# Performance work log

Measured on AMD Instinct MI355X. Metric: run time of the kernel, lower is better.

Reference implementation:

```python
import jax, jax.numpy as jnp
import numpy as np

TEM_PER_GROUP = 4  # arg_split: templates per argument type


def setup_inputs() -> dict:
    key = jax.random.key(0)
    k1, k2, k3, k4, k5 = jax.random.split(key, 5)
    B, L, D, S, G = 8, 4096, 768, 32, 16
    T = G * TEM_PER_GROUP
    return {
        "sen_embs": jax.random.normal(k1, (B, L, D), dtype=jnp.float32),
        "arg_embs": jax.random.normal(k2, (B, S, T, D), dtype=jnp.float32),
        "mask_type": jax.random.uniform(k3, (B, S, G), dtype=jnp.float32),
        "span_start": jax.random.randint(k4, (B, S), 0, 4000),
        "span_len": jax.random.randint(k5, (B, S), 1, 20),
        "offset": 10,
    }


def reference(sen_embs, arg_embs, mask_type, span_start, span_len, offset):
    B, L, D = sen_embs.shape
    _, S, T, _ = arg_embs.shape
    G = T // TEM_PER_GROUP
    # variable-length span gather + mean pool (sen_emb[max(0,s-off):e+1+off].mean(0))
    lo = jnp.maximum(span_start - offset, 0)                       # [B,S]
    hi = jnp.minimum(span_start + span_len + 1 + offset, L)       # [B,S]
    pos = jnp.arange(L)
    m = ((pos[None, None, :] >= lo[:, :, None]) &
         (pos[None, None, :] < hi[:, :, None])).astype(sen_embs.dtype)  # [B,S,L]
    cnt = jnp.maximum(m.sum(-1), 1.0)                              # [B,S]
    span = jnp.einsum('bsl,bld->bsd', m, sen_embs) / cnt[:, :, None]    # [B,S,D]
    # similarity (dis='ou'): -||arg - span||^2 over feature dim
    diff = arg_embs - span[:, :, None, :]                          # [B,S,T,D]
    logits = -(diff * diff).sum(-1)                                # [B,S,T]
    # segmented max over template groups (torch.split + max)
    logits = logits.reshape(B, S, G, TEM_PER_GROUP).max(-1)        # [B,S,G]
    return logits * mask_type
```

## Files before the change

### kernel.cpp

```cpp
#include <hip/hip_runtime.h>

constexpr int B   = 8;
constexpr int L   = 4096;
constexpr int D   = 768;
constexpr int S   = 32;
constexpr int G   = 16;
constexpr int TPG = 4;
constexpr int T   = G * TPG;

__global__ __launch_bounds__(256) void span_sim_kernel(
    const float* __restrict__ sen,
    const float* __restrict__ arg,
    const float* __restrict__ mask,
    const int*   __restrict__ sstart,
    const int*   __restrict__ slen,
    const int*   __restrict__ offp,
    float*       __restrict__ out)
{
    const int bs   = blockIdx.x;
    const int b    = bs / S;
    const int tid  = threadIdx.x;
    const int lane = tid & 63;
    const int wave = tid >> 6;

    const int offset = offp[0];
    const int st = sstart[bs];
    const int ln = slen[bs];
    int lo = st - offset;           if (lo < 0) lo = 0;
    int hi = st + ln + 1 + offset;  if (hi > L) hi = L;
    const int cnt = hi - lo;

    __shared__ float span[D];

    const float* srow = sen + ((size_t)b * L + lo) * D;
    float a0 = 0.f, a1 = 0.f, a2 = 0.f;
    #pragma unroll 4
    for (int r = 0; r < cnt; ++r) {
        const float* p = srow + (size_t)r * D;
        a0 += p[tid];
        a1 += p[tid + 256];
        a2 += p[tid + 512];
    }
    const float inv = 1.0f / (float)cnt;
    span[tid]       = a0 * inv;
    span[tid + 256] = a1 * inv;
    span[tid + 512] = a2 * inv;
    __syncthreads();

    const float4* sp4 = reinterpret_cast<const float4*>(span);
    const float4 s0 = sp4[lane];
    const float4 s1 = sp4[lane + 64];
    const float4 s2 = sp4[lane + 128];

    const float4* abase = reinterpret_cast<const float4*>(arg + (size_t)bs * T * D);
    float gmax[4];
    #pragma unroll
    for (int i = 0; i < 16; ++i) {
        const int t = wave * 16 + i;
        const float4* a4 = abase + (size_t)t * (D / 4);
        const float4 v0 = a4[lane];
        const float4 v1 = a4[lane + 64];
        const float4 v2 = a4[lane + 128];
        float d = 0.f, x;
        x = v0.x - s0.x; d += x * x;  x = v0.y - s0.y; d += x * x;
        x = v0.z - s0.z; d += x * x;  x = v0.w - s0.w; d += x * x;
        x = v1.x - s1.x; d += x * x;  x = v1.y - s1.y; d += x * x;
        x = v1.z - s1.z; d += x * x;  x = v1.w - s1.w; d += x * x;
        x = v2.x - s2.x; d += x * x;  x = v2.y - s2.y; d += x * x;
        x = v2.z - s2.z; d += x * x;  x = v2.w - s2.w; d += x * x;
        #pragma unroll
        for (int o = 32; o >= 1; o >>= 1) d += __shfl_xor(d, o, 64);
        const float lg = -d;
        const int j = i >> 2;
        if ((i & 3) == 0) gmax[j] = lg;
        else              gmax[j] = fmaxf(gmax[j], lg);
    }

    if (lane == 0) {
        float*       o  = out  + (size_t)bs * G + wave * 4;
        const float* mk = mask + (size_t)bs * G + wave * 4;
        o[0] = gmax[0] * mk[0];
        o[1] = gmax[1] * mk[1];
        o[2] = gmax[2] * mk[2];
        o[3] = gmax[3] * mk[3];
    }
}

extern "C" void kernel_launch(void* const* d_in, const int* in_sizes, int n_in,
                              void* d_out, int out_size, void* d_ws, size_t ws_size,
                              hipStream_t stream) {
    const float* sen    = (const float*)d_in[0];
    const float* arg    = (const float*)d_in[1];
    const float* mask   = (const float*)d_in[2];
    const int*   sstart = (const int*)d_in[3];
    const int*   slen   = (const int*)d_in[4];
    const int*   offp   = (const int*)d_in[5];
    float*       out    = (float*)d_out;

    span_sim_kernel<<<B * S, 256, 0, stream>>>(sen, arg, mask, sstart, slen, offp, out);
}
```

Before: 172.4 us.

## Use 1024-thread blocks, splitting span rows and templates across more waves

After: 171.4 us. No clear change (-0.6%).

```diff
diff --git a/kernel.cpp b/kernel.cpp
--- a/kernel.cpp
+++ b/kernel.cpp
@@ -8,7 +8,7 @@
 constexpr int TPG = 4;
 constexpr int T   = G * TPG;
 
-__global__ __launch_bounds__(256) void span_sim_kernel(
+__global__ __launch_bounds__(1024) void span_sim_kernel(
     const float* __restrict__ sen,
     const float* __restrict__ arg,
     const float* __restrict__ mask,
@@ -18,7 +18,7 @@
     float*       __restrict__ out)
 {
     const int bs   = blockIdx.x;
-    const int b    = bs / S;
+    const int b    = bs >> 5;
     const int tid  = threadIdx.x;
     const int lane = tid & 63;
     const int wave = tid >> 6;
@@ -30,21 +30,33 @@
     int hi = st + ln + 1 + offset;  if (hi > L) hi = L;
     const int cnt = hi - lo;
 
+    __shared__ float part[4][D];
     __shared__ float span[D];
 
+    const int c  = tid & 255;
+    const int rq = tid >> 8;
     const float* srow = sen + ((size_t)b * L + lo) * D;
     float a0 = 0.f, a1 = 0.f, a2 = 0.f;
     #pragma unroll 4
-    for (int r = 0; r < cnt; ++r) {
+    for (int r = rq; r < cnt; r += 4) {
         const float* p = srow + (size_t)r * D;
-        a0 += p[tid];
-        a1 += p[tid + 256];
-        a2 += p[tid + 512];
+        a0 += p[c];
+        a1 += p[c + 256];
+        a2 += p[c + 512];
     }
-    const float inv = 1.0f / (float)cnt;
-    span[tid]       = a0 * inv;
-    span[tid + 256] = a1 * inv;
-    span[tid + 512] = a2 * inv;
+    part[rq][c]       = a0;
+    part[rq][c + 256] = a1;
+    part[rq][c + 512] = a2;
+    __syncthreads();
+
+    if (tid < 256) {
+        const float inv = 1.0f / (float)cnt;
+        #pragma unroll
+        for (int k = 0; k < 3; ++k) {
+            const int j = tid + k * 256;
+            span[j] = (part[0][j] + part[1][j] + part[2][j] + part[3][j]) * inv;
+        }
+    }
     __syncthreads();
 
     const float4* sp4 = reinterpret_cast<const float4*>(span);
@@ -53,11 +65,10 @@
     const float4 s2 = sp4[lane + 128];
 
     const float4* abase = reinterpret_cast<const float4*>(arg + (size_t)bs * T * D);
-    float gmax[4];
+    float dist[4];
     #pragma unroll
-    for (int i = 0; i < 16; ++i) {
-        const int t = wave * 16 + i;
-        const float4* a4 = abase + (size_t)t * (D / 4);
+    for (int i = 0; i < 4; ++i) {
+        const float4* a4 = abase + (size_t)(wave * 4 + i) * (D / 4);
         const float4 v0 = a4[lane];
         const float4 v1 = a4[lane + 64];
         const float4 v2 = a4[lane + 128];
@@ -68,21 +79,16 @@
         x = v1.z - s1.z; d += x * x;  x = v1.w - s1.w; d += x * x;
         x = v2.x - s2.x; d += x * x;  x = v2.y - s2.y; d += x * x;
         x = v2.z - s2.z; d += x * x;  x = v2.w - s2.w; d += x * x;
+        dist[i] = d;
+    }
+    #pragma unroll
+    for (int o = 32; o >= 1; o >>= 1) {
         #pragma unroll
-        for (int o = 32; o >= 1; o >>= 1) d += __shfl_xor(d, o, 64);
-        const float lg = -d;
-        const int j = i >> 2;
-        if ((i & 3) == 0) gmax[j] = lg;
-        else              gmax[j] = fmaxf(gmax[j], lg);
+        for (int i = 0; i < 4; ++i) dist[i] += __shfl_xor(dist[i], o, 64);
     }
-
     if (lane == 0) {
-        float*       o  = out  + (size_t)bs * G + wave * 4;
-        const float* mk = mask + (size_t)bs * G + wave * 4;
-        o[0] = gmax[0] * mk[0];
-        o[1] = gmax[1] * mk[1];
-        o[2] = gmax[2] * mk[2];
-        o[3] = gmax[3] * mk[3];
+        const float m = fmaxf(fmaxf(-dist[0], -dist[1]), fmaxf(-dist[2], -dist[3]));
+        out[(size_t)bs * G + wave] = m * mask[(size_t)bs * G + wave];
     }
 }
 
@@ -97,5 +103,5 @@
     const int*   offp   = (const int*)d_in[5];
     float*       out    = (float*)d_out;
 
-    span_sim_kernel<<<B * S, 256, 0, stream>>>(sen, arg, mask, sstart, slen, offp, out);
+    span_sim_kernel<<<B * S, 1024, 0, stream>>>(sen, arg, mask, sstart, slen, offp, out);
 }
```
